# Optimization experiments

Hardware: AMD Instinct MI355X
Metric: run time of the kernel (lower is better)

Reference implementation:

```python
import jax, jax.numpy as jnp
import numpy as np

N, E, H, L, T = 20000, 160000, 128, 4, 20


def _ln(x, g, b):
    m = jnp.mean(x, -1, keepdims=True)
    v = jnp.mean((x - m) ** 2, -1, keepdims=True)
    return (x - m) * jax.lax.rsqrt(v + 1e-5) * g + b


def _mlp(x, W1, b1, W2, b2, g, b):
    # Linear -> ReLU -> Linear -> LayerNorm, as in mlp_2layer
    h = jax.nn.relu(x @ W1 + b1)
    return _ln(h @ W2 + b2, g, b)


def setup_inputs() -> dict:
    key = jax.random.key(0)
    ks = iter(jax.random.split(key, 64))

    def W(shape):
        fan_in = shape[-2]
        return jax.random.normal(next(ks), shape, jnp.float32) * (fan_in ** -0.5)

    z = lambda s: jnp.zeros(s, jnp.float32)
    o = lambda s: jnp.ones(s, jnp.float32)

    inp = {
        'x': jax.random.normal(next(ks), (N, 12), jnp.float32),
        'edge_attr': jax.random.normal(next(ks), (E, 4), jnp.float32),
        'edge_index': jax.random.randint(next(ks), (2, E), 0, N),
        # node encoder (12 -> H)
        'Wn1': W((12, H)), 'bn1': z((H,)), 'Wn2': W((H, H)), 'bn2': z((H,)), 'gn_ln': o((H,)), 'bn_ln': z((H,)),
        # edge encoder (4 -> H)
        'We1': W((4, H)), 'be1': z((H,)), 'We2': W((H, H)), 'be2': z((H,)), 'ge_ln': o((H,)), 'be_ln': z((H,)),
        # stacked per-layer params: edge_mlp (4H -> H), node_mlp (3H -> H), global_mlp (3H -> H)
        'lEW1': W((L, 4 * H, H)), 'lEb1': z((L, H)), 'lEW2': W((L, H, H)), 'lEb2': z((L, H)), 'lEg': o((L, H)), 'lEbt': z((L, H)),
        'lVW1': W((L, 3 * H, H)), 'lVb1': z((L, H)), 'lVW2': W((L, H, H)), 'lVb2': z((L, H)), 'lVg': o((L, H)), 'lVbt': z((L, H)),
        'lGW1': W((L, 3 * H, H)), 'lGb1': z((L, H)), 'lGW2': W((L, H, H)), 'lGb2': z((L, H)), 'lGg': o((L, H)), 'lGbt': z((L, H)),
        # CNN output head: Conv1d(1->8,k=15,s=4) -> ReLU -> Conv1d(8->1,k=10,s=1)
        'c1w': jax.random.normal(next(ks), (8, 1, 15), jnp.float32) * 0.1, 'c1b': z((8,)),
        'c2w': jax.random.normal(next(ks), (1, 8, 10), jnp.float32) * 0.1, 'c2b': z((1,)),
    }
    return inp


def _forward(x, edge_attr, edge_index,
             Wn1, bn1, Wn2, bn2, gn_ln, bn_ln,
             We1, be1, We2, be2, ge_ln, be_ln,
             lEW1, lEb1, lEW2, lEb2, lEg, lEbt,
             lVW1, lVb1, lVW2, lVb2, lVg, lVbt,
             lGW1, lGb1, lGW2, lGb2, lGg, lGbt,
             c1w, c1b, c2w, c2b):
    senders = edge_index[0]
    receivers = edge_index[1]
    n_nodes = x.shape[0]
    n_edges = edge_attr.shape[0]

    x_v = _mlp(x, Wn1, bn1, Wn2, bn2, gn_ln, bn_ln)          # [N, H]
    x_e = _mlp(edge_attr, We1, be1, We2, be2, ge_ln, be_ln)  # [E, H]
    g = jnp.zeros((1, H), x_v.dtype)                          # B=1 global (no global inputs)

    def step(carry, p):
        x_v, x_e, g = carry
        (EW1, Eb1, EW2, Eb2, Eg, Ebt,
         VW1, Vb1, VW2, Vb2, Vg, Vbt,
         GW1, Gb1, GW2, Gb2, Gg, Gbt) = p
        # edge update: gather sender/receiver feats, concat with edge + global
        g_e = jnp.broadcast_to(g, (n_edges, H))
        edge_in = jnp.concatenate([x_v[senders], x_v[receivers], x_e, g_e], -1)  # [E, 4H]
        x_e = x_e + _mlp(edge_in, EW1, Eb1, EW2, Eb2, Eg, Ebt)
        # node update: sum-aggregate messages by receiver
        aggr = jax.ops.segment_sum(x_e, receivers, num_segments=n_nodes)  # [N, H]
        g_v = jnp.broadcast_to(g, (n_nodes, H))
        node_in = jnp.concatenate([x_v, aggr, g_v], -1)  # [N, 3H]
        x_v = x_v + _mlp(node_in, VW1, Vb1, VW2, Vb2, Vg, Vbt)
        # global update
        g_in = jnp.concatenate([jnp.sum(x_v, 0, keepdims=True), jnp.sum(x_e, 0, keepdims=True), g], -1)  # [1, 3H]
        g = g + _mlp(g_in, GW1, Gb1, GW2, Gb2, Gg, Gbt)
        return (x_v, x_e, g), None

    params = (lEW1, lEb1, lEW2, lEb2, lEg, lEbt,
              lVW1, lVb1, lVW2, lVb2, lVg, lVbt,
              lGW1, lGb1, lGW2, lGb2, lGg, lGbt)
    (x_v, x_e, g), _ = jax.lax.scan(step, (x_v, x_e, g), params)

    # CNN head over the H=128 feature axis -> [N, T]
    dn = ('NCH', 'OIH', 'NCH')
    h = x_v[:, None, :]  # [N, 1, 128]
    h = jax.lax.conv_general_dilated(h, c1w, (4,), 'VALID', dimension_numbers=dn)
    h = jax.nn.relu(h + c1b[None, :, None])  # [N, 8, 29]
    h = jax.lax.conv_general_dilated(h, c2w, (1,), 'VALID', dimension_numbers=dn) + c2b[None, :, None]
    return h[:, 0, :]  # [N, 20]


def reference(x, edge_attr, edge_index,
              Wn1, bn1, Wn2, bn2, gn_ln, bn_ln,
              We1, be1, We2, be2, ge_ln, be_ln,
              lEW1, lEb1, lEW2, lEb2, lEg, lEbt,
              lVW1, lVb1, lVW2, lVb2, lVg, lVbt,
              lGW1, lGb1, lGW2, lGb2, lGg, lGbt,
              c1w, c1b, c2w, c2b):
    return _forward(x, edge_attr, edge_index,
                    Wn1, bn1, Wn2, bn2, gn_ln, bn_ln,
                    We1, be1, We2, be2, ge_ln, be_ln,
                    lEW1, lEb1, lEW2, lEb2, lEg, lEbt,
                    lVW1, lVb1, lVW2, lVb2, lVg, lVbt,
                    lGW1, lGb1, lGW2, lGb2, lGg, lGbt,
                    c1w, c1b, c2w, c2b)
```

## Files before the change

### kernel.cpp

```cpp
#include <hip/hip_runtime.h>

#define NN 20000
#define NE 160000
#define HD 128
#define SA 136

typedef __attribute__((ext_vector_type(8))) short  bfrag;
typedef __attribute__((ext_vector_type(4))) float  facc;
typedef __attribute__((ext_vector_type(4))) float  f4v;

__device__ __forceinline__ float bf2f(unsigned short u){
  union { unsigned int i; float f; } v; v.i = ((unsigned int)u) << 16; return v.f;
}
__device__ __forceinline__ unsigned short f2bf(float f){
  union { float f; unsigned int i; } v; v.f = f;
  unsigned int r = v.i + 0x7fffu + ((v.i >> 16) & 1u);
  return (unsigned short)(r >> 16);
}

__global__ void sentinel_kernel(float* out, float code){
  if (threadIdx.x < 32) out[threadIdx.x] = code;
}

__device__ __forceinline__ void gemm_tile(const short* Ab,
                                          const unsigned short* pk,
                                          int m0, int lane, facc acc[8]){
  const int q = lane >> 4, c = lane & 15;
  #pragma unroll
  for (int kt = 0; kt < 4; ++kt){
    bfrag a = *(const bfrag*)(Ab + (m0 + c) * SA + kt * 32 + q * 8);
    const bfrag* bp = (const bfrag*)pk + kt * 512 + lane;
    #pragma unroll
    for (int nt = 0; nt < 8; ++nt){
      acc[nt] = __builtin_amdgcn_mfma_f32_16x16x32_bf16(a, bp[nt * 64], acc[nt], 0, 0, 0);
    }
  }
}

__global__ __launch_bounds__(256) void pack_all(
    const float* Wn2, const float* We2,
    const float* lEW1, const float* lEW2,
    const float* lVW1, const float* lVW2,
    unsigned short* packed)
{
  int job = blockIdx.x * 256 + threadIdx.x;
  int mat = job >> 12, r12 = job & 4095;
  int plane = r12 >> 11, r = r12 & 2047;
  int kt = r >> 9, nt = (r >> 6) & 7, lane = r & 63;
  const float* src;
  if (mat == 0) src = Wn2;
  else if (mat == 1) src = We2;
  else {
    int m2 = mat - 2, l = m2 / 7, t = m2 % 7;
    switch (t){
      case 0: src = lEW1 + ((size_t)l*512 +   0)*HD; break;
      case 1: src = lEW1 + ((size_t)l*512 + 128)*HD; break;
      case 2: src = lEW1 + ((size_t)l*512 + 256)*HD; break;
      case 3: src = lEW2 + (size_t)l*HD*HD;          break;
      case 4: src = lVW1 + ((size_t)l*384 +   0)*HD; break;
      case 5: src = lVW1 + ((size_t)l*384 + 128)*HD; break;
      default: src = lVW2 + (size_t)l*HD*HD;         break;
    }
  }
  int krow = kt*32 + (lane>>4)*8, col = nt*16 + (lane&15);
  unsigned short v[8];
  #pragma unroll
  for (int j = 0; j < 8; ++j){
    float w = src[(size_t)(krow + j)*HD + col];
    unsigned short h = f2bf(w);
    v[j] = plane ? f2bf(w - bf2f(h)) : h;
  }
  unsigned short* dst = packed + ((size_t)mat*2 + plane)*16384
                               + ((size_t)(kt*8+nt)*64 + lane)*8;
  #pragma unroll
  for (int j = 0; j < 8; ++j) dst[j] = v[j];
}

__global__ __launch_bounds__(128) void init_small(
    float* g, float* cbe, float* cbv, float* xvs, float* xes,
    const float* Eb1_0, const float* Vb1_0)
{
  int t = threadIdx.x;
  g[t] = 0.f; xvs[t] = 0.f; xes[t] = 0.f;
  cbe[t] = Eb1_0[t]; cbv[t] = Vb1_0[t];
}

__global__ __launch_bounds__(256) void zero_cnt(int* cnt){
  int i = blockIdx.x * 256 + threadIdx.x;
  if (i < NN) cnt[i] = 0;
}
__global__ __launch_bounds__(256) void hist_kernel(const int* eidx, int* cnt){
  int e = blockIdx.x * 256 + threadIdx.x;
  atomicAdd(&cnt[eidx[NE + e]], 1);
}
__global__ __launch_bounds__(1024) void scan_kernel(const int* cnt, int* base, int* ofs){
  __shared__ int wsum[16];
  int t = threadIdx.x, lane = t & 63;
  int vals[20]; int loc = 0;
  if (t < 1000){
    #pragma unroll
    for (int k = 0; k < 20; ++k){ vals[k] = cnt[t*20 + k]; loc += vals[k]; }
  }
  int inc = loc;
  #pragma unroll
  for (int d = 1; d < 64; d <<= 1){ int o = __shfl_up(inc, d); if (lane >= d) inc += o; }
  if (lane == 63) wsum[t >> 6] = inc;
  __syncthreads();
  if (t < 16){
    int v = wsum[t];
    #pragma unroll
    for (int d = 1; d < 16; d <<= 1){ int o = __shfl_up(v, d); if (t >= d) v += o; }
    wsum[t] = v;
  }
  __syncthreads();
  int woff = (t >= 64) ? wsum[(t >> 6) - 1] : 0;
  int run = woff + inc - loc;
  if (t < 1000){
    #pragma unroll
    for (int k = 0; k < 20; ++k){ base[t*20 + k] = run; ofs[t*20 + k] = run; run += vals[k]; }
  }
  if (t == 0) base[NN] = NE;
}
__global__ __launch_bounds__(256) void scatter_kernel(const int* eidx, int* ofs,
                                                      int* perm, int* ssid, int* srid){
  int e = blockIdx.x * 256 + threadIdx.x;
  int s = eidx[e], r = eidx[NE + e];
  int pos = atomicAdd(&ofs[r], 1);
  perm[pos] = e; ssid[pos] = s; srid[pos] = r;
}

__global__ __launch_bounds__(256) void enc_node(
    const float* x, const float* W1, const float* b1,
    const unsigned short* pkW2, const float* b2,
    const float* gl, const float* bl, float* xvf, int nrows)
{
  __shared__ float inb[64*12];
  __shared__ __align__(16) short Hh[64*SA];
  __shared__ __align__(16) short Hl[64*SA];
  int tid = threadIdx.x, r0 = blockIdx.x * 64;
  for (int j = tid; j < 64*12; j += 256){
    int rr = j / 12, k = j % 12, rg = r0 + rr;
    inb[j] = (rg < nrows) ? x[(size_t)rg*12 + k] : 0.f;
  }
  __syncthreads();
  {
    int cc = tid & 127;
    float w1c[12];
    #pragma unroll
    for (int k = 0; k < 12; ++k) w1c[k] = W1[k*HD + cc];
    float bb = b1[cc];
    for (int it = 0; it < 32; ++it){
      int rr = it*2 + (tid >> 7);
      float a = bb;
      #pragma unroll
      for (int k = 0; k < 12; ++k) a += inb[rr*12 + k] * w1c[k];
      float h = fmaxf(a, 0.f);
      unsigned short hh = f2bf(h);
      Hh[rr*SA + cc] = (short)hh;
      Hl[rr*SA + cc] = (short)f2bf(h - bf2f(hh));
    }
  }
  __syncthreads();
  int lane = tid & 63, q = lane >> 4, c = lane & 15, m0 = (tid >> 6) * 16;
  facc a2[8];
  #pragma unroll
  for (int nt = 0; nt < 8; ++nt) a2[nt] = (facc){0.f,0.f,0.f,0.f};
  gemm_tile(Hh, pkW2,         m0, lane, a2);
  gemm_tile(Hl, pkW2,         m0, lane, a2);
  gemm_tile(Hh, pkW2 + 16384, m0, lane, a2);
  #pragma unroll
  for (int i = 0; i < 4; ++i){
    int rl = m0 + q*4 + i, rg = r0 + rl;
    float vals[8], s = 0.f, ss = 0.f;
    #pragma unroll
    for (int nt = 0; nt < 8; ++nt){
      float v = a2[nt][i] + b2[nt*16 + c];
      vals[nt] = v; s += v; ss += v*v;
    }
    s += __shfl_xor(s,1); ss += __shfl_xor(ss,1);
    s += __shfl_xor(s,2); ss += __shfl_xor(ss,2);
    s += __shfl_xor(s,4); ss += __shfl_xor(ss,4);
    s += __shfl_xor(s,8); ss += __shfl_xor(ss,8);
    float mean = s * 0.0078125f;
    float var  = ss * 0.0078125f - mean*mean;
    float rs   = rsqrtf(var + 1e-5f);
    if (rg < nrows){
      #pragma unroll
      for (int nt = 0; nt < 8; ++nt){
        int col = nt*16 + c;
        xvf[(size_t)rg*HD + col] = (vals[nt]-mean)*rs*gl[col] + bl[col];
      }
    }
  }
}

__global__ __launch_bounds__(256) void enc_edge(
    const float* ea, const int* perm, const float* W1, const float* b1,
    const unsigned short* pkW2, const float* b2,
    const float* gl, const float* bl, unsigned short* xeb)
{
  __shared__ float inb[64*4];
  __shared__ __align__(16) short Hh[64*SA];
  __shared__ __align__(16) short Hl[64*SA];
  int tid = threadIdx.x, r0 = blockIdx.x * 64;
  {
    int rr = tid >> 2, k = tid & 3;
    int pe = perm[r0 + rr];
    inb[tid] = ea[(size_t)pe*4 + k];
  }
  __syncthreads();
  {
    int cc = tid & 127;
    float w0 = W1[0*HD+cc], w1 = W1[1*HD+cc], w2 = W1[2*HD+cc], w3 = W1[3*HD+cc];
    float bb = b1[cc];
    for (int it = 0; it < 32; ++it){
      int rr = it*2 + (tid >> 7);
      float a = bb + inb[rr*4+0]*w0 + inb[rr*4+1]*w1 + inb[rr*4+2]*w2 + inb[rr*4+3]*w3;
      float h = fmaxf(a, 0.f);
      unsigned short hh = f2bf(h);
      Hh[rr*SA + cc] = (short)hh;
      Hl[rr*SA + cc] = (short)f2bf(h - bf2f(hh));
    }
  }
  __syncthreads();
  int lane = tid & 63, q = lane >> 4, c = lane & 15, m0 = (tid >> 6) * 16;
  facc a2[8];
  #pragma unroll
  for (int nt = 0; nt < 8; ++nt) a2[nt] = (facc){0.f,0.f,0.f,0.f};
  gemm_tile(Hh, pkW2,         m0, lane, a2);
  gemm_tile(Hl, pkW2,         m0, lane, a2);
  gemm_tile(Hh, pkW2 + 16384, m0, lane, a2);
  #pragma unroll
  for (int i = 0; i < 4; ++i){
    int rl = m0 + q*4 + i, rg = r0 + rl;
    float vals[8], s = 0.f, ss = 0.f;
    #pragma unroll
    for (int nt = 0; nt < 8; ++nt){
      float v = a2[nt][i] + b2[nt*16 + c];
      vals[nt] = v; s += v; ss += v*v;
    }
    s += __shfl_xor(s,1); ss += __shfl_xor(ss,1);
    s += __shfl_xor(s,2); ss += __shfl_xor(ss,2);
    s += __shfl_xor(s,4); ss += __shfl_xor(ss,4);
    s += __shfl_xor(s,8); ss += __shfl_xor(ss,8);
    float mean = s * 0.0078125f;
    float var  = ss * 0.0078125f - mean*mean;
    float rs   = rsqrtf(var + 1e-5f);
    #pragma unroll
    for (int nt = 0; nt < 8; ++nt){
      int col = nt*16 + c;
      xeb[(size_t)rg*HD + col] = f2bf((vals[nt]-mean)*rs*gl[col] + bl[col]);
    }
  }
}

__global__ __launch_bounds__(256) void pq_kernel(
    const float* xvf, const unsigned short* pkA, const unsigned short* pkB,
    unsigned short* P, unsigned short* Q, int nrows)
{
  __shared__ __align__(16) short Ah[64*SA];
  __shared__ __align__(16) short Al[64*SA];
  int tid = threadIdx.x, r0 = blockIdx.x * 64;
  for (int j = tid; j < 1024; j += 256){
    int rr = j >> 4, ch = j & 15, rg = r0 + rr;
    float v[8];
    if (rg < nrows){
      f4v a = *(const f4v*)(xvf + (size_t)rg*HD + ch*8);
      f4v b = *(const f4v*)(xvf + (size_t)rg*HD + ch*8 + 4);
      v[0]=a[0];v[1]=a[1];v[2]=a[2];v[3]=a[3];v[4]=b[0];v[5]=b[1];v[6]=b[2];v[7]=b[3];
    } else {
      #pragma unroll
      for (int k = 0; k < 8; ++k) v[k] = 0.f;
    }
    short* dh = Ah + rr*SA + ch*8;
    short* dl = Al + rr*SA + ch*8;
    #pragma unroll
    for (int k = 0; k < 8; ++k){
      unsigned short h = f2bf(v[k]);
      dh[k] = (short)h; dl[k] = (short)f2bf(v[k] - bf2f(h));
    }
  }
  __syncthreads();
  int lane = tid & 63, q = lane >> 4, c = lane & 15, m0 = (tid >> 6) * 16;
  facc ap[8], aq[8];
  #pragma unroll
  for (int nt = 0; nt < 8; ++nt){ ap[nt] = (facc){0.f,0.f,0.f,0.f}; aq[nt] = (facc){0.f,0.f,0.f,0.f}; }
  gemm_tile(Ah, pkA,         m0, lane, ap);
  gemm_tile(Al, pkA,         m0, lane, ap);
  gemm_tile(Ah, pkA + 16384, m0, lane, ap);
  gemm_tile(Ah, pkB,         m0, lane, aq);
  gemm_tile(Al, pkB,         m0, lane, aq);
  gemm_tile(Ah, pkB + 16384, m0, lane, aq);
  #pragma unroll
  for (int i = 0; i < 4; ++i){
    int rl = m0 + q*4 + i, rg = r0 + rl;
    if (rg < nrows){
      bfrag pv, qv;
      #pragma unroll
      for (int nt = 0; nt < 8; ++nt){
        pv[nt] = (short)f2bf(ap[nt][i]);
        qv[nt] = (short)f2bf(aq[nt][i]);
      }
      *(bfrag*)(P + (size_t)rg*HD + c*8) = pv;
      *(bfrag*)(Q + (size_t)rg*HD + c*8) = qv;
    }
  }
}

__global__ __launch_bounds__(256) void edge_kernel(
    unsigned short* xeb, const int* ssid, const int* srid,
    const unsigned short* P, const unsigned short* Q, const float* cbe,
    const unsigned short* pkW1c, const unsigned short* pkW2,
    const float* Eb2, const float* Eg, const float* Ebt)
{
  __shared__ __align__(16) short Ab[64*SA];
  __shared__ __align__(16) short Hh[64*SA];
  __shared__ __align__(16) short Hl[64*SA];
  __shared__ int sidx[64], ridx[64];
  int tid = threadIdx.x, e0 = blockIdx.x * 64;
  for (int j = tid; j < 1024; j += 256){
    int rr = j >> 4, ch = j & 15;
    *(bfrag*)(Ab + rr*SA + ch*8) = *(const bfrag*)(xeb + (size_t)(e0+rr)*HD + ch*8);
  }
  if (tid < 64){ sidx[tid] = ssid[e0+tid]; ridx[tid] = srid[e0+tid]; }
  __syncthreads();
  int lane = tid & 63, q = lane >> 4, c = lane & 15, m0 = (tid >> 6) * 16;
  float cb[8];
  #pragma unroll
  for (int nt = 0; nt < 8; ++nt) cb[nt] = cbe[nt*16 + c];
  float pg[4][8];
  #pragma unroll
  for (int i = 0; i < 4; ++i){
    int rl = m0 + q*4 + i;
    bfrag ps = *(const bfrag*)(P + (size_t)sidx[rl]*HD + c*8);
    bfrag qr = *(const bfrag*)(Q + (size_t)ridx[rl]*HD + c*8);
    #pragma unroll
    for (int nt = 0; nt < 8; ++nt)
      pg[i][nt] = bf2f((unsigned short)ps[nt]) + bf2f((unsigned short)qr[nt]) + cb[nt];
  }
  facc acc[8];
  #pragma unroll
  for (int nt = 0; nt < 8; ++nt) acc[nt] = (facc){0.f,0.f,0.f,0.f};
  gemm_tile(Ab, pkW1c,         m0, lane, acc);
  gemm_tile(Ab, pkW1c + 16384, m0, lane, acc);
  #pragma unroll
  for (int i = 0; i < 4; ++i){
    int rl = m0 + q*4 + i;
    #pragma unroll
    for (int nt = 0; nt < 8; ++nt){
      int col = nt*16 + c;
      float h = fmaxf(acc[nt][i] + pg[i][nt], 0.f);
      unsigned short hh = f2bf(h);
      Hh[rl*SA + col] = (short)hh;
      Hl[rl*SA + col] = (short)f2bf(h - bf2f(hh));
    }
  }
  __syncthreads();
  facc a2[8];
  #pragma unroll
  for (int nt = 0; nt < 8; ++nt) a2[nt] = (facc){0.f,0.f,0.f,0.f};
  gemm_tile(Hh, pkW2,         m0, lane, a2);
  gemm_tile(Hl, pkW2,         m0, lane, a2);
  gemm_tile(Hh, pkW2 + 16384, m0, lane, a2);
  #pragma unroll
  for (int i = 0; i < 4; ++i){
    int rl = m0 + q*4 + i, eg = e0 + rl;
    float vals[8], s = 0.f, ss = 0.f;
    #pragma unroll
    for (int nt = 0; nt < 8; ++nt){
      float v = a2[nt][i] + Eb2[nt*16 + c];
      vals[nt] = v; s += v; ss += v*v;
    }
    s += __shfl_xor(s,1); ss += __shfl_xor(ss,1);
    s += __shfl_xor(s,2); ss += __shfl_xor(ss,2);
    s += __shfl_xor(s,4); ss += __shfl_xor(ss,4);
    s += __shfl_xor(s,8); ss += __shfl_xor(ss,8);
    float mean = s * 0.0078125f;
    float var  = ss * 0.0078125f - mean*mean;
    float rs   = rsqrtf(var + 1e-5f);
    #pragma unroll
    for (int nt = 0; nt < 8; ++nt){
      int col = nt*16 + c;
      float o = (vals[nt]-mean)*rs*Eg[col] + Ebt[col];
      float nv = bf2f((unsigned short)Ab[rl*SA + col]) + o;
      xeb[(size_t)eg*HD + col] = f2bf(nv);
    }
  }
}

__global__ __launch_bounds__(256) void aggr_kernel(
    const unsigned short* xeb, const int* base, float* aggr, float* xes, int do_xes)
{
  __shared__ float red[128];
  int tid = threadIdx.x, lane = tid & 63, wq = tid >> 6;
  if (tid < 128) red[tid] = 0.f;
  __syncthreads();
  float xp0 = 0.f, xp1 = 0.f;
  int n0 = blockIdx.x * 32 + wq * 8;
  for (int j = 0; j < 8; ++j){
    int n = n0 + j;
    int b0 = base[n], b1 = base[n + 1];
    float s0 = 0.f, s1 = 0.f;
    int e = b0;
    for (; e + 1 < b1; e += 2){
      unsigned int u0 = *(const unsigned int*)(xeb + (size_t)e*HD + lane*2);
      unsigned int u1 = *(const unsigned int*)(xeb + (size_t)(e+1)*HD + lane*2);
      s0 += bf2f((unsigned short)(u0 & 0xffffu)) + bf2f((unsigned short)(u1 & 0xffffu));
      s1 += bf2f((unsigned short)(u0 >> 16))     + bf2f((unsigned short)(u1 >> 16));
    }
    if (e < b1){
      unsigned int u0 = *(const unsigned int*)(xeb + (size_t)e*HD + lane*2);
      s0 += bf2f((unsigned short)(u0 & 0xffffu));
      s1 += bf2f((unsigned short)(u0 >> 16));
    }
    float2 o; o.x = s0; o.y = s1;
    *(float2*)(aggr + (size_t)n*HD + lane*2) = o;
    xp0 += s0; xp1 += s1;
  }
  if (do_xes){
    atomicAdd(&red[lane*2],     xp0);
    atomicAdd(&red[lane*2 + 1], xp1);
    __syncthreads();
    if (tid < 128) atomicAdd(&xes[tid], red[tid]);
  }
}

__global__ __launch_bounds__(256) void node_kernel(
    float* xvf, const float* aggr, const float* cbv,
    const unsigned short* pkW1a, const unsigned short* pkW1b, const unsigned short* pkW2,
    const float* Vb2, const float* Vg, const float* Vbt,
    float* xv_sum, int nrows)
{
  __shared__ __align__(16) short Avh[64*SA];
  __shared__ __align__(16) short Avl[64*SA];
  __shared__ __align__(16) short Agh[64*SA];
  __shared__ __align__(16) short Agl[64*SA];
  int tid = threadIdx.x, r0 = blockIdx.x * 64;
  for (int j = tid; j < 1024; j += 256){
    int rr = j >> 4, ch = j & 15, rg = r0 + rr;
    float v[8], w[8];
    if (rg < nrows){
      f4v a = *(const f4v*)(xvf  + (size_t)rg*HD + ch*8);
      f4v b = *(const f4v*)(xvf  + (size_t)rg*HD + ch*8 + 4);
      f4v e = *(const f4v*)(aggr + (size_t)rg*HD + ch*8);
      f4v f = *(const f4v*)(aggr + (size_t)rg*HD + ch*8 + 4);
      v[0]=a[0];v[1]=a[1];v[2]=a[2];v[3]=a[3];v[4]=b[0];v[5]=b[1];v[6]=b[2];v[7]=b[3];
      w[0]=e[0];w[1]=e[1];w[2]=e[2];w[3]=e[3];w[4]=f[0];w[5]=f[1];w[6]=f[2];w[7]=f[3];
    } else {
      #pragma unroll
      for (int k = 0; k < 8; ++k){ v[k]=0.f; w[k]=0.f; }
    }
    short *dvh = Avh + rr*SA + ch*8, *dvl = Avl + rr*SA + ch*8;
    short *dgh = Agh + rr*SA + ch*8, *dgl = Agl + rr*SA + ch*8;
    #pragma unroll
    for (int k = 0; k < 8; ++k){
      unsigned short h1 = f2bf(v[k]);
      dvh[k] = (short)h1; dvl[k] = (short)f2bf(v[k] - bf2f(h1));
      unsigned short h2 = f2bf(w[k]);
      dgh[k] = (short)h2; dgl[k] = (short)f2bf(w[k] - bf2f(h2));
    }
  }
  __syncthreads();
  int lane = tid & 63, q = lane >> 4, c = lane & 15, m0 = (tid >> 6) * 16;
  facc acc[8];
  #pragma unroll
  for (int nt = 0; nt < 8; ++nt) acc[nt] = (facc){0.f,0.f,0.f,0.f};
  gemm_tile(Avh, pkW1a,         m0, lane, acc);
  gemm_tile(Avl, pkW1a,         m0, lane, acc);
  gemm_tile(Avh, pkW1a + 16384, m0, lane, acc);
  gemm_tile(Agh, pkW1b,         m0, lane, acc);
  gemm_tile(Agl, pkW1b,         m0, lane, acc);
  gemm_tile(Agh, pkW1b + 16384, m0, lane, acc);
  __syncthreads();
  #pragma unroll
  for (int i = 0; i < 4; ++i){
    int rl = m0 + q*4 + i;
    #pragma unroll
    for (int nt = 0; nt < 8; ++nt){
      int col = nt*16 + c;
      float h = fmaxf(acc[nt][i] + cbv[col], 0.f);
      unsigned short hh = f2bf(h);
      Avh[rl*SA + col] = (short)hh;
      Avl[rl*SA + col] = (short)f2bf(h - bf2f(hh));
    }
  }
  __syncthreads();
  facc a2[8];
  #pragma unroll
  for (int nt = 0; nt < 8; ++nt) a2[nt] = (facc){0.f,0.f,0.f,0.f};
  gemm_tile(Avh, pkW2,         m0, lane, a2);
  gemm_tile(Avl, pkW2,         m0, lane, a2);
  gemm_tile(Avh, pkW2 + 16384, m0, lane, a2);
  float csum[8] = {0.f,0.f,0.f,0.f,0.f,0.f,0.f,0.f};
  #pragma unroll
  for (int i = 0; i < 4; ++i){
    int rl = m0 + q*4 + i, rg = r0 + rl;
    bool ok = rg < nrows;
    float vals[8], s = 0.f, ss = 0.f;
    #pragma unroll
    for (int nt = 0; nt < 8; ++nt){
      float v = a2[nt][i] + Vb2[nt*16 + c];
      vals[nt] = v; s += v; ss += v*v;
    }
    s += __shfl_xor(s,1); ss += __shfl_xor(ss,1);
    s += __shfl_xor(s,2); ss += __shfl_xor(ss,2);
    s += __shfl_xor(s,4); ss += __shfl_xor(ss,4);
    s += __shfl_xor(s,8); ss += __shfl_xor(ss,8);
    float mean = s * 0.0078125f;
    float var  = ss * 0.0078125f - mean*mean;
    float rs   = rsqrtf(var + 1e-5f);
    if (ok){
      #pragma unroll
      for (int nt = 0; nt < 8; ++nt){
        int col = nt*16 + c;
        float o = (vals[nt]-mean)*rs*Vg[col] + Vbt[col];
        size_t gi = (size_t)rg*HD + col;
        float nv = xvf[gi] + o;
        xvf[gi] = nv;
        csum[nt] += nv;
      }
    }
  }
  #pragma unroll
  for (int nt = 0; nt < 8; ++nt){
    float v = csum[nt]; v += __shfl_xor(v,16); v += __shfl_xor(v,32);
    if (q == 0) atomicAdd(&xv_sum[nt*16 + c], v);
  }
}

__global__ __launch_bounds__(128) void g_kernel(
    float* xvs, float* xes, float* g,
    const float* GW1, const float* Gb1, const float* GW2, const float* Gb2,
    const float* Gg, const float* Gbt,
    float* cbe, float* cbv,
    const float* EW1n, const float* Eb1n, const float* VW1n, const float* Vb1n)
{
  __shared__ float gin[384], h1[128], gn[128], red[4];
  int t = threadIdx.x;
  gin[t] = xvs[t]; gin[128 + t] = xes[t]; gin[256 + t] = g[t];
  __syncthreads();
  float a = Gb1[t];
  for (int k = 0; k < 384; ++k) a += gin[k] * GW1[(size_t)k*HD + t];
  h1[t] = fmaxf(a, 0.f);
  __syncthreads();
  float o = Gb2[t];
  for (int k = 0; k < 128; ++k) o += h1[k] * GW2[(size_t)k*HD + t];
  float s = o;
  #pragma unroll
  for (int d = 1; d < 64; d <<= 1) s += __shfl_xor(s, d);
  if ((t & 63) == 0) red[t >> 6] = s;
  __syncthreads();
  float mean = (red[0] + red[1]) * 0.0078125f;
  float dd = o - mean;
  float v = dd * dd;
  #pragma unroll
  for (int d = 1; d < 64; d <<= 1) v += __shfl_xor(v, d);
  if ((t & 63) == 0) red[2 + (t >> 6)] = v;
  __syncthreads();
  float rs = rsqrtf((red[2] + red[3]) * 0.0078125f + 1e-5f);
  float gnv = g[t] + (o - mean)*rs*Gg[t] + Gbt[t];
  g[t] = gnv; gn[t] = gnv;
  xvs[t] = 0.f; xes[t] = 0.f;
  __syncthreads();
  float ce = Eb1n[t], cv = Vb1n[t];
  for (int k = 0; k < 128; ++k){
    ce += gn[k] * EW1n[(size_t)k*HD + t];
    cv += gn[k] * VW1n[(size_t)k*HD + t];
  }
  cbe[t] = ce; cbv[t] = cv;
}

__global__ __launch_bounds__(256) void decoder_kernel(
    const float* xv, const float* c1w, const float* c1b,
    const float* c2w, const float* c2b, float* out)
{
  __shared__ float xl[4][128];
  __shared__ float hl[4][232];
  __shared__ float w1[120], b1[8], w2[80];
  __shared__ float b2s;
  int tid = threadIdx.x, nl = tid >> 6, t = tid & 63;
  int n = blockIdx.x * 4 + nl;
  if (tid < 120) w1[tid] = c1w[tid];
  else if (tid < 128) b1[tid - 120] = c1b[tid - 120];
  else if (tid < 208) w2[tid - 128] = c2w[tid - 128];
  else if (tid == 208) b2s = c2b[0];
  xl[nl][t]      = xv[(size_t)n*HD + t];
  xl[nl][t + 64] = xv[(size_t)n*HD + 64 + t];
  __syncthreads();
  for (int j = t; j < 232; j += 64){
    int ch = j / 29, pp = j % 29;
    float a = b1[ch];
    #pragma unroll
    for (int u = 0; u < 15; ++u) a += xl[nl][4*pp + u] * w1[ch*15 + u];
    hl[nl][j] = fmaxf(a, 0.f);
  }
  __syncthreads();
  if (t < 20){
    float o = b2s;
    #pragma unroll
    for (int ch = 0; ch < 8; ++ch)
      #pragma unroll
      for (int u = 0; u < 10; ++u)
        o += hl[nl][ch*29 + t + u] * w2[ch*10 + u];
    out[(size_t)n*20 + t] = o;
  }
}

extern "C" void kernel_launch(void* const* d_in, const int* in_sizes, int n_in,
                              void* d_out, int out_size, void* d_ws, size_t ws_size,
                              hipStream_t stream)
{
  const float* x    = (const float*)d_in[0];
  const float* ea   = (const float*)d_in[1];
  const int*   eidx = (const int*)d_in[2];
  const float* Wn1  = (const float*)d_in[3];  const float* bn1  = (const float*)d_in[4];
  const float* Wn2  = (const float*)d_in[5];  const float* bn2  = (const float*)d_in[6];
  const float* gnln = (const float*)d_in[7];  const float* bnln = (const float*)d_in[8];
  const float* We1  = (const float*)d_in[9];  const float* be1  = (const float*)d_in[10];
  const float* We2  = (const float*)d_in[11]; const float* be2  = (const float*)d_in[12];
  const float* geln = (const float*)d_in[13]; const float* beln = (const float*)d_in[14];
  const float* lEW1 = (const float*)d_in[15]; const float* lEb1 = (const float*)d_in[16];
  const float* lEW2 = (const float*)d_in[17]; const float* lEb2 = (const float*)d_in[18];
  const float* lEg  = (const float*)d_in[19]; const float* lEbt = (const float*)d_in[20];
  const float* lVW1 = (const float*)d_in[21]; const float* lVb1 = (const float*)d_in[22];
  const float* lVW2 = (const float*)d_in[23]; const float* lVb2 = (const float*)d_in[24];
  const float* lVg  = (const float*)d_in[25]; const float* lVbt = (const float*)d_in[26];
  const float* lGW1 = (const float*)d_in[27]; const float* lGb1 = (const float*)d_in[28];
  const float* lGW2 = (const float*)d_in[29]; const float* lGb2 = (const float*)d_in[30];
  const float* lGg  = (const float*)d_in[31]; const float* lGbt = (const float*)d_in[32];
  const float* c1w  = (const float*)d_in[33]; const float* c1b  = (const float*)d_in[34];
  const float* c2w  = (const float*)d_in[35]; const float* c2b  = (const float*)d_in[36];

  char* ws = (char*)d_ws;
  size_t off = 0;
  auto alloc = [&](size_t b){ size_t o = off; off += (b + 255) & ~(size_t)255; return o; };
  unsigned short* pk   = (unsigned short*)(ws + alloc((size_t)30*2*16384*2));
  float*          g    = (float*)(ws + alloc(512));
  float*          cbe  = (float*)(ws + alloc(512));
  float*          cbv  = (float*)(ws + alloc(512));
  float*          xvs  = (float*)(ws + alloc(512));
  float*          xes  = (float*)(ws + alloc(512));
  float*          xvf  = (float*)(ws + alloc((size_t)NN*HD*4));
  unsigned short* P    = (unsigned short*)(ws + alloc((size_t)NN*HD*2));
  unsigned short* Q    = (unsigned short*)(ws + alloc((size_t)NN*HD*2));
  float*          aggr = (float*)(ws + alloc((size_t)NN*HD*4));
  unsigned short* xeb  = (unsigned short*)(ws + alloc((size_t)NE*HD*2));
  int*            cnt  = (int*)(ws + alloc((size_t)NN*4));
  int*            bse  = (int*)(ws + alloc((size_t)(NN+1)*4));
  int*            ofs  = (int*)(ws + alloc((size_t)NN*4));
  int*            perm = (int*)(ws + alloc((size_t)NE*4));
  int*            ssid = (int*)(ws + alloc((size_t)NE*4));
  int*            srid = (int*)(ws + alloc((size_t)NE*4));

  if (ws_size < off){
    sentinel_kernel<<<1, 32, 0, stream>>>((float*)d_out, 20000.f + (float)(ws_size >> 20));
    return;
  }

  auto slot = [&](int m){ return pk + (size_t)m * 32768; };

  pack_all<<<480, 256, 0, stream>>>(Wn2, We2, lEW1, lEW2, lVW1, lVW2, pk);
  init_small<<<1, 128, 0, stream>>>(g, cbe, cbv, xvs, xes, lEb1, lVb1);
  zero_cnt<<<(NN + 255)/256, 256, 0, stream>>>(cnt);
  hist_kernel<<<NE/256, 256, 0, stream>>>(eidx, cnt);
  scan_kernel<<<1, 1024, 0, stream>>>(cnt, bse, ofs);
  scatter_kernel<<<NE/256, 256, 0, stream>>>(eidx, ofs, perm, ssid, srid);

  enc_node<<<(NN + 63)/64, 256, 0, stream>>>(x, Wn1, bn1, slot(0), bn2, gnln, bnln, xvf, NN);
  enc_edge<<<NE/64, 256, 0, stream>>>(ea, perm, We1, be1, slot(1), be2, geln, beln, xeb);

  for (int l = 0; l < 4; ++l){
    int m = 2 + 7*l;
    pq_kernel<<<(NN + 63)/64, 256, 0, stream>>>(xvf, slot(m+0), slot(m+1), P, Q, NN);
    edge_kernel<<<NE/64, 256, 0, stream>>>(xeb, ssid, srid, P, Q, cbe,
        slot(m+2), slot(m+3),
        lEb2 + (size_t)l*HD, lEg + (size_t)l*HD, lEbt + (size_t)l*HD);
    aggr_kernel<<<NN/32, 256, 0, stream>>>(xeb, bse, aggr, xes, (l < 3) ? 1 : 0);
    node_kernel<<<(NN + 63)/64, 256, 0, stream>>>(xvf, aggr, cbv,
        slot(m+4), slot(m+5), slot(m+6),
        lVb2 + (size_t)l*HD, lVg + (size_t)l*HD, lVbt + (size_t)l*HD,
        xvs, NN);
    if (l < 3){
      g_kernel<<<1, 128, 0, stream>>>(xvs, xes, g,
          lGW1 + (size_t)l*384*HD, lGb1 + (size_t)l*HD,
          lGW2 + (size_t)l*HD*HD, lGb2 + (size_t)l*HD,
          lGg + (size_t)l*HD, lGbt + (size_t)l*HD,
          cbe, cbv,
          lEW1 + ((size_t)(l+1)*512 + 384)*HD, lEb1 + (size_t)(l+1)*HD,
          lVW1 + ((size_t)(l+1)*384 + 256)*HD, lVb1 + (size_t)(l+1)*HD);
    }
  }
  decoder_kernel<<<NN/4, 256, 0, stream>>>(xvf, c1w, c1b, c2w, c2b, (float*)d_out);

  hipError_t e = hipGetLastError();
  if (e != hipSuccess){
    sentinel_kernel<<<1, 32, 0, stream>>>((float*)d_out, 10000.f + (float)e);
  }
  (void)in_sizes; (void)n_in; (void)out_size;
}
```

Before: 964.4 us.

## Fuse edge aggregation into node kernel and parallelize global MLP over 1024 threads

The separate aggregation kernel is removed. The node kernel now gathers each node's incoming edge features straight from the CSR-ordered edge buffer and writes the bf16 hi/lo split directly into shared memory, which drops the fp32 aggr round trip through global memory and one launch per layer. The single-block global MLP kernel moves from 128 to 1024 threads, splitting each dot-product K range into 8 partial sums that are reduced through shared memory, to shorten that serial step. The risk is that node blocks, with 313 blocks of 64 rows, now carry the irregular gather latency and get less parallelism for it than the old 625-block aggregation grid.

```diff
diff --git a/kernel.cpp b/kernel.cpp
--- a/kernel.cpp
+++ b/kernel.cpp
@@ -388,80 +388,70 @@
   }
 }
 
-__global__ __launch_bounds__(256) void aggr_kernel(
-    const unsigned short* xeb, const int* base, float* aggr, float* xes, int do_xes)
-{
-  __shared__ float red[128];
-  int tid = threadIdx.x, lane = tid & 63, wq = tid >> 6;
-  if (tid < 128) red[tid] = 0.f;
-  __syncthreads();
-  float xp0 = 0.f, xp1 = 0.f;
-  int n0 = blockIdx.x * 32 + wq * 8;
-  for (int j = 0; j < 8; ++j){
-    int n = n0 + j;
-    int b0 = base[n], b1 = base[n + 1];
-    float s0 = 0.f, s1 = 0.f;
-    int e = b0;
-    for (; e + 1 < b1; e += 2){
-      unsigned int u0 = *(const unsigned int*)(xeb + (size_t)e*HD + lane*2);
-      unsigned int u1 = *(const unsigned int*)(xeb + (size_t)(e+1)*HD + lane*2);
-      s0 += bf2f((unsigned short)(u0 & 0xffffu)) + bf2f((unsigned short)(u1 & 0xffffu));
-      s1 += bf2f((unsigned short)(u0 >> 16))     + bf2f((unsigned short)(u1 >> 16));
-    }
-    if (e < b1){
-      unsigned int u0 = *(const unsigned int*)(xeb + (size_t)e*HD + lane*2);
-      s0 += bf2f((unsigned short)(u0 & 0xffffu));
-      s1 += bf2f((unsigned short)(u0 >> 16));
-    }
-    float2 o; o.x = s0; o.y = s1;
-    *(float2*)(aggr + (size_t)n*HD + lane*2) = o;
-    xp0 += s0; xp1 += s1;
-  }
-  if (do_xes){
-    atomicAdd(&red[lane*2],     xp0);
-    atomicAdd(&red[lane*2 + 1], xp1);
-    __syncthreads();
-    if (tid < 128) atomicAdd(&xes[tid], red[tid]);
-  }
-}
-
 __global__ __launch_bounds__(256) void node_kernel(
-    float* xvf, const float* aggr, const float* cbv,
+    float* xvf, const unsigned short* xeb, const int* base, const float* cbv,
     const unsigned short* pkW1a, const unsigned short* pkW1b, const unsigned short* pkW2,
     const float* Vb2, const float* Vg, const float* Vbt,
-    float* xv_sum, int nrows)
+    float* xv_sum, float* xes, int do_xes, int nrows)
 {
   __shared__ __align__(16) short Avh[64*SA];
   __shared__ __align__(16) short Avl[64*SA];
   __shared__ __align__(16) short Agh[64*SA];
   __shared__ __align__(16) short Agl[64*SA];
+  __shared__ float red[128];
   int tid = threadIdx.x, r0 = blockIdx.x * 64;
+  int lane = tid & 63, wq = tid >> 6;
+  if (tid < 128) red[tid] = 0.f;
   for (int j = tid; j < 1024; j += 256){
     int rr = j >> 4, ch = j & 15, rg = r0 + rr;
-    float v[8], w[8];
+    float v[8];
     if (rg < nrows){
-      f4v a = *(const f4v*)(xvf  + (size_t)rg*HD + ch*8);
-      f4v b = *(const f4v*)(xvf  + (size_t)rg*HD + ch*8 + 4);
-      f4v e = *(const f4v*)(aggr + (size_t)rg*HD + ch*8);
-      f4v f = *(const f4v*)(aggr + (size_t)rg*HD + ch*8 + 4);
+      f4v a = *(const f4v*)(xvf + (size_t)rg*HD + ch*8);
+      f4v b = *(const f4v*)(xvf + (size_t)rg*HD + ch*8 + 4);
       v[0]=a[0];v[1]=a[1];v[2]=a[2];v[3]=a[3];v[4]=b[0];v[5]=b[1];v[6]=b[2];v[7]=b[3];
-      w[0]=e[0];w[1]=e[1];w[2]=e[2];w[3]=e[3];w[4]=f[0];w[5]=f[1];w[6]=f[2];w[7]=f[3];
     } else {
       #pragma unroll
-      for (int k = 0; k < 8; ++k){ v[k]=0.f; w[k]=0.f; }
+      for (int k = 0; k < 8; ++k) v[k] = 0.f;
     }
     short *dvh = Avh + rr*SA + ch*8, *dvl = Avl + rr*SA + ch*8;
-    short *dgh = Agh + rr*SA + ch*8, *dgl = Agl + rr*SA + ch*8;
     #pragma unroll
     for (int k = 0; k < 8; ++k){
       unsigned short h1 = f2bf(v[k]);
       dvh[k] = (short)h1; dvl[k] = (short)f2bf(v[k] - bf2f(h1));
-      unsigned short h2 = f2bf(w[k]);
-      dgh[k] = (short)h2; dgl[k] = (short)f2bf(w[k] - bf2f(h2));
-    }
-  }
-  __syncthreads();
-  int lane = tid & 63, q = lane >> 4, c = lane & 15, m0 = (tid >> 6) * 16;
+    }
+  }
+  float xp0 = 0.f, xp1 = 0.f;
+  for (int j = 0; j < 16; ++j){
+    int rl = wq*16 + j, rg = r0 + rl;
+    float s0 = 0.f, s1 = 0.f;
+    if (rg < nrows){
+      int b0 = base[rg], b1 = base[rg + 1];
+      int e = b0;
+      for (; e + 1 < b1; e += 2){
+        unsigned int u0 = *(const unsigned int*)(xeb + (size_t)e*HD + lane*2);
+        unsigned int u1 = *(const unsigned int*)(xeb + (size_t)(e+1)*HD + lane*2);
+        s0 += bf2f((unsigned short)(u0 & 0xffffu)) + bf2f((unsigned short)(u1 & 0xffffu));
+        s1 += bf2f((unsigned short)(u0 >> 16))     + bf2f((unsigned short)(u1 >> 16));
+      }
+      if (e < b1){
+        unsigned int u0 = *(const unsigned int*)(xeb + (size_t)e*HD + lane*2);
+        s0 += bf2f((unsigned short)(u0 & 0xffffu));
+        s1 += bf2f((unsigned short)(u0 >> 16));
+      }
+    }
+    unsigned short h0 = f2bf(s0), h1 = f2bf(s1);
+    unsigned short l0 = f2bf(s0 - bf2f(h0)), l1 = f2bf(s1 - bf2f(h1));
+    *(unsigned int*)(Agh + rl*SA + 2*lane) = ((unsigned int)h1 << 16) | h0;
+    *(unsigned int*)(Agl + rl*SA + 2*lane) = ((unsigned int)l1 << 16) | l0;
+    xp0 += s0; xp1 += s1;
+  }
+  if (do_xes){
+    atomicAdd(&red[lane*2],     xp0);
+    atomicAdd(&red[lane*2 + 1], xp1);
+  }
+  __syncthreads();
+  if (do_xes && tid < 128) atomicAdd(&xes[tid], red[tid]);
+  int q = lane >> 4, c = lane & 15, m0 = (tid >> 6) * 16;
   facc acc[8];
   #pragma unroll
   for (int nt = 0; nt < 8; ++nt) acc[nt] = (facc){0.f,0.f,0.f,0.f};
@@ -528,7 +518,7 @@
   }
 }
 
-__global__ __launch_bounds__(128) void g_kernel(
+__global__ __launch_bounds__(1024) void g_kernel(
     float* xvs, float* xes, float* g,
     const float* GW1, const float* Gb1, const float* GW2, const float* Gb2,
     const float* Gg, const float* Gbt,
@@ -536,38 +526,74 @@
     const float* EW1n, const float* Eb1n, const float* VW1n, const float* Vb1n)
 {
   __shared__ float gin[384], h1[128], gn[128], red[4];
-  int t = threadIdx.x;
-  gin[t] = xvs[t]; gin[128 + t] = xes[t]; gin[256 + t] = g[t];
-  __syncthreads();
-  float a = Gb1[t];
-  for (int k = 0; k < 384; ++k) a += gin[k] * GW1[(size_t)k*HD + t];
-  h1[t] = fmaxf(a, 0.f);
-  __syncthreads();
-  float o = Gb2[t];
-  for (int k = 0; k < 128; ++k) o += h1[k] * GW2[(size_t)k*HD + t];
-  float s = o;
-  #pragma unroll
-  for (int d = 1; d < 64; d <<= 1) s += __shfl_xor(s, d);
-  if ((t & 63) == 0) red[t >> 6] = s;
+  __shared__ float partA[8][128], partB[8][128];
+  int tid = threadIdx.x, t = tid & 127, kk = tid >> 7;
+  if (tid < 384) gin[tid] = (tid < 128) ? xvs[tid] : (tid < 256) ? xes[tid-128] : g[tid-256];
+  __syncthreads();
+  {
+    float a = 0.f;
+    for (int k = kk*48; k < kk*48 + 48; ++k) a += gin[k] * GW1[(size_t)k*HD + t];
+    partA[kk][t] = a;
+  }
+  __syncthreads();
+  if (kk == 0){
+    float a = Gb1[t];
+    #pragma unroll
+    for (int i = 0; i < 8; ++i) a += partA[i][t];
+    h1[t] = fmaxf(a, 0.f);
+  }
+  __syncthreads();
+  {
+    float o = 0.f;
+    for (int k = kk*16; k < kk*16 + 16; ++k) o += h1[k] * GW2[(size_t)k*HD + t];
+    partA[kk][t] = o;
+  }
+  __syncthreads();
+  float oo = 0.f;
+  if (kk == 0){
+    oo = Gb2[t];
+    #pragma unroll
+    for (int i = 0; i < 8; ++i) oo += partA[i][t];
+  }
+  __syncthreads();
+  if (tid < 128){
+    float s = oo;
+    #pragma unroll
+    for (int d = 1; d < 64; d <<= 1) s += __shfl_xor(s, d);
+    if ((tid & 63) == 0) red[tid >> 6] = s;
+  }
   __syncthreads();
   float mean = (red[0] + red[1]) * 0.0078125f;
-  float dd = o - mean;
-  float v = dd * dd;
-  #pragma unroll
-  for (int d = 1; d < 64; d <<= 1) v += __shfl_xor(v, d);
-  if ((t & 63) == 0) red[2 + (t >> 6)] = v;
-  __syncthreads();
-  float rs = rsqrtf((red[2] + red[3]) * 0.0078125f + 1e-5f);
-  float gnv = g[t] + (o - mean)*rs*Gg[t] + Gbt[t];
-  g[t] = gnv; gn[t] = gnv;
-  xvs[t] = 0.f; xes[t] = 0.f;
-  __syncthreads();
-  float ce = Eb1n[t], cv = Vb1n[t];
-  for (int k = 0; k < 128; ++k){
-    ce += gn[k] * EW1n[(size_t)k*HD + t];
-    cv += gn[k] * VW1n[(size_t)k*HD + t];
-  }
-  cbe[t] = ce; cbv[t] = cv;
+  if (tid < 128){
+    float dd = oo - mean;
+    float v = dd * dd;
+    #pragma unroll
+    for (int d = 1; d < 64; d <<= 1) v += __shfl_xor(v, d);
+    if ((tid & 63) == 0) red[2 + (tid >> 6)] = v;
+  }
+  __syncthreads();
+  if (tid < 128){
+    float rs = rsqrtf((red[2] + red[3]) * 0.0078125f + 1e-5f);
+    float gnv = g[tid] + (oo - mean)*rs*Gg[tid] + Gbt[tid];
+    g[tid] = gnv; gn[tid] = gnv;
+    xvs[tid] = 0.f; xes[tid] = 0.f;
+  }
+  __syncthreads();
+  {
+    float ce = 0.f, cv = 0.f;
+    for (int k = kk*16; k < kk*16 + 16; ++k){
+      ce += gn[k] * EW1n[(size_t)k*HD + t];
+      cv += gn[k] * VW1n[(size_t)k*HD + t];
+    }
+    partA[kk][t] = ce; partB[kk][t] = cv;
+  }
+  __syncthreads();
+  if (kk == 0){
+    float ce = Eb1n[t], cv = Vb1n[t];
+    #pragma unroll
+    for (int i = 0; i < 8; ++i){ ce += partA[i][t]; cv += partB[i][t]; }
+    cbe[t] = ce; cbv[t] = cv;
+  }
 }
 
 __global__ __launch_bounds__(256) void decoder_kernel(
@@ -643,7 +669,6 @@
   float*          xvf  = (float*)(ws + alloc((size_t)NN*HD*4));
   unsigned short* P    = (unsigned short*)(ws + alloc((size_t)NN*HD*2));
   unsigned short* Q    = (unsigned short*)(ws + alloc((size_t)NN*HD*2));
-  float*          aggr = (float*)(ws + alloc((size_t)NN*HD*4));
   unsigned short* xeb  = (unsigned short*)(ws + alloc((size_t)NE*HD*2));
   int*            cnt  = (int*)(ws + alloc((size_t)NN*4));
   int*            bse  = (int*)(ws + alloc((size_t)(NN+1)*4));
@@ -675,13 +700,12 @@
     edge_kernel<<<NE/64, 256, 0, stream>>>(xeb, ssid, srid, P, Q, cbe,
         slot(m+2), slot(m+3),
         lEb2 + (size_t)l*HD, lEg + (size_t)l*HD, lEbt + (size_t)l*HD);
-    aggr_kernel<<<NN/32, 256, 0, stream>>>(xeb, bse, aggr, xes, (l < 3) ? 1 : 0);
-    node_kernel<<<(NN + 63)/64, 256, 0, stream>>>(xvf, aggr, cbv,
+    node_kernel<<<(NN + 63)/64, 256, 0, stream>>>(xvf, xeb, bse, cbv,
         slot(m+4), slot(m+5), slot(m+6),
         lVb2 + (size_t)l*HD, lVg + (size_t)l*HD, lVbt + (size_t)l*HD,
-        xvs, NN);
+        xvs, xes, (l < 3) ? 1 : 0, NN);
     if (l < 3){
-      g_kernel<<<1, 128, 0, stream>>>(xvs, xes, g,
+      g_kernel<<<1, 1024, 0, stream>>>(xvs, xes, g,
           lGW1 + (size_t)l*384*HD, lGb1 + (size_t)l*HD,
           lGW2 + (size_t)l*HD*HD, lGb2 + (size_t)l*HD,
           lGg + (size_t)l*HD, lGbt + (size_t)l*HD,
```

After: 913.9 us. 5.2% less time.
